# Optimization experiments

Hardware: AMD Instinct MI355X
Metric: run time of the kernel (lower is better)

## Reference

```python
import jax, jax.numpy as jnp
import numpy as np

# Model dims (Gemma-class)
B, T, HID = 1, 3072, 2048
H, KH, D = 16, 8, 128          # q heads, kv heads, head_dim
WIN = 1024                     # sliding window
EPS = 1e-6
SEQ = 1536                     # two packed sequences of length 1536


def _rms(x, w):
    # torch nn.RMSNorm: x * rsqrt(mean(x^2) + eps) [* weight]
    var = jnp.mean(x * x, axis=-1, keepdims=True)
    y = x * jax.lax.rsqrt(var + EPS)
    return y if w is None else y * w


def _rotate_half(x):
    x1, x2 = jnp.split(x, 2, axis=-1)
    return jnp.concatenate([-x2, x1], axis=-1)


def _rope(x, cos, sin):
    # x: [B,T,h,D]; cos/sin: [B,T,rd] -> unsqueeze head dim (matches cos.unsqueeze(2))
    c = cos[:, :, None, :]
    s = sin[:, :, None, :]
    rd = cos.shape[-1]
    xr, xp = x[..., :rd], x[..., rd:]
    xr = xr * c + _rotate_half(xr) * s
    return jnp.concatenate([xr, xp], axis=-1)


def _build_mask(cu_seqlens):
    # causal & within sliding window & same packed sequence (matches _sliding_mask)
    idx = jnp.arange(T)
    seg = jnp.searchsorted(cu_seqlens, idx, side='right') - 1
    i = idx[:, None]
    j = idx[None, :]
    return (i >= j) & ((i - j) < WIN) & (seg[:, None] == seg[None, :])


def _attn_layer(x, wq, qn, k, v, wo, cos, sin, mask):
    # x: [B,T,HID]; k,v: [T,KH,D] (possibly shared from an earlier layer)
    q = _rope(_rms((x @ wq).reshape(B, T, H, D), qn), cos, sin).reshape(T, H, D)
    rep = H // k.shape[1]
    kk = jnp.repeat(k, rep, axis=1)   # GQA: repeat_interleave over head dim
    vv = jnp.repeat(v, rep, axis=1)
    s = jnp.einsum('qhd,khd->hqk', q, kk)          # scale = 1.0 (as in source)
    s = jnp.where(mask, s, jnp.asarray(-1e30, s.dtype))
    p = jax.nn.softmax(s, axis=-1)
    o = jnp.einsum('hqk,khd->qhd', p, vv).reshape(B, T, H * D)
    return o @ wo


def setup_inputs() -> dict:
    key = jax.random.key(0)
    ks = jax.random.split(key, 10)
    hidden_states = jax.random.normal(ks[0], (B, T, HID), jnp.float32)
    # RoPE tables with per-packed-sequence position resets
    pos = jnp.concatenate([jnp.arange(SEQ), jnp.arange(SEQ)]).astype(jnp.float32)
    inv = 1.0 / (10000.0 ** (jnp.arange(0, D, 2, dtype=jnp.float32) / D))
    fr = pos[:, None] * inv[None, :]
    emb = jnp.concatenate([fr, fr], axis=-1)     # [T, D]
    cos = jnp.cos(emb)[None]                     # [1, T, D]
    sin = jnp.sin(emb)[None]
    w = lambda k, sh: 0.02 * jax.random.normal(k, sh, jnp.float32)
    return {
        'hidden_states': hidden_states,
        'cos': cos, 'sin': sin,
        'wq0': w(ks[1], (HID, H * D)), 'wk0': w(ks[2], (HID, KH * D)),
        'wv0': w(ks[3], (HID, KH * D)), 'wo0': w(ks[4], (H * D, HID)),
        'qn0': 1.0 + 0.01 * jax.random.normal(ks[5], (D,), jnp.float32),
        'kn0': 1.0 + 0.01 * jax.random.normal(ks[6], (D,), jnp.float32),
        'wq1': w(ks[7], (HID, H * D)), 'wo1': w(ks[8], (H * D, HID)),
        'qn1': 1.0 + 0.01 * jax.random.normal(ks[9], (D,), jnp.float32),
        'cu_seqlens': jnp.array([0, SEQ, T], dtype=jnp.int32),
    }


def reference(hidden_states, cos, sin, wq0, wk0, wv0, wo0, qn0, kn0, wq1, wo1, qn1, cu_seqlens):
    mask = _build_mask(cu_seqlens)
    # Layer 0: source layer -> computes and stores K/V
    k = _rope(_rms((hidden_states @ wk0).reshape(B, T, KH, D), kn0), cos, sin).reshape(T, KH, D)
    v = _rms((hidden_states @ wv0).reshape(B, T, KH, D), None).reshape(T, KH, D)
    out0 = _attn_layer(hidden_states, wq0, qn0, k, v, wo0, cos, sin, mask)
    # Layer 1: KV-shared layer -> reuses layer 0's K/V (skips k/v projections)
    out1 = _attn_layer(out0, wq1, qn1, k, v, wo1, cos, sin, mask)
    return out1
```

## Files before the change

kernel.cpp:

```cpp
#include <hip/hip_runtime.h>
#include <hip/hip_bf16.h>

#define T_TOK 3072
#define HIDDEN 2048
#define NHQ 16
#define NHKV 8
#define DH 128
#define WINDOW 1024
#define KVN 1024

typedef __attribute__((ext_vector_type(4))) float f32x4;
typedef __attribute__((ext_vector_type(8))) short bf16x8;
typedef __attribute__((ext_vector_type(8))) unsigned short ushort8;
typedef __attribute__((ext_vector_type(4))) unsigned short ushort4v;

__device__ __forceinline__ unsigned short f2bf(float f) {
  union { float fv; unsigned u; } v; v.fv = f;
  unsigned r = v.u + 0x7fffu + ((v.u >> 16) & 1u);
  return (unsigned short)(r >> 16);
}
__device__ __forceinline__ float bf2f(unsigned short h) {
  union { unsigned u; float f; } v; v.u = ((unsigned)h) << 16;
  return v.f;
}
__device__ __forceinline__ void split2(float f, unsigned short& hi, unsigned short& lo) {
  hi = f2bf(f);
  lo = f2bf(f - bf2f(hi));
}

__global__ __launch_bounds__(256) void prep(const float* __restrict__ hidden,
                                            const float* __restrict__ wq0,
                                            const float* __restrict__ wk0,
                                            const float* __restrict__ wv0,
                                            const float* __restrict__ wo0,
                                            const float* __restrict__ wq1,
                                            const float* __restrict__ wo1,
                                            unsigned short* __restrict__ xh,
                                            unsigned short* __restrict__ xl,
                                            unsigned short* __restrict__ wqkvh,
                                            unsigned short* __restrict__ wqkvl,
                                            unsigned short* __restrict__ wo0sh,
                                            unsigned short* __restrict__ wo0sl,
                                            unsigned short* __restrict__ wq1th,
                                            unsigned short* __restrict__ wq1tl,
                                            unsigned short* __restrict__ wo1th) {
  __shared__ float tile[32][33];
  const int K = HIDDEN;
  int id = blockIdx.x;
  if (id < 6144 || (id >= 14336 && id < 18432)) {
    const float* src; unsigned short *dh, *dl; int local;
    if (id < 6144) { src = hidden; dh = xh; dl = xl; local = id; }
    else           { src = wo0; dh = wo0sh; dl = wo0sl; local = id - 14336; }
    int i = (local * 256 + threadIdx.x) * 4;
    f32x4 v = *(const f32x4*)(src + i);
    ushort4v oh, ol;
#pragma unroll
    for (int j = 0; j < 4; ++j) {
      unsigned short h, l;
      split2(v[j], h, l);
      oh[j] = h; ol[j] = l;
    }
    *(ushort4v*)(dh + i) = oh;
    *(ushort4v*)(dl + i) = ol;
    return;
  }
  const float* W; int N, local; unsigned short *Dh, *Dl; size_t dstoff;
  if (id < 14336) {
    int lid = id - 6144;
    if (lid < 4096)      { W = wq0; N = 2048; local = lid;        dstoff = 0; }
    else if (lid < 6144) { W = wk0; N = 1024; local = lid - 4096; dstoff = (size_t)2048 * K; }
    else                 { W = wv0; N = 1024; local = lid - 6144; dstoff = (size_t)3072 * K; }
    Dh = wqkvh; Dl = wqkvl;
  } else if (id < 22528) {
    W = wq1; N = 2048; local = id - 18432; dstoff = 0;
    Dh = wq1th; Dl = wq1tl;
  } else {
    W = wo1; N = 2048; local = id - 22528; dstoff = 0;
    Dh = wo1th; Dl = nullptr;
  }
  int ntc = N / 32;
  int bn = (local % ntc) * 32, bk = (local / ntc) * 32;
  int tx = threadIdx.x & 31, ty = threadIdx.x >> 5;
#pragma unroll
  for (int i = 0; i < 4; ++i)
    tile[ty + i * 8][tx] = W[(size_t)(bk + ty + i * 8) * N + bn + tx];
  __syncthreads();
#pragma unroll
  for (int i = 0; i < 4; ++i) {
    unsigned short h, l;
    split2(tile[tx][ty + i * 8], h, l);
    Dh[dstoff + (size_t)(bn + ty + i * 8) * K + bk + tx] = h;
    if (Dl) Dl[dstoff + (size_t)(bn + ty + i * 8) * K + bk + tx] = l;
  }
}

__global__ __launch_bounds__(256) void transpose_u16(const unsigned short* __restrict__ src,
                                                     unsigned short* __restrict__ dst,
                                                     int R, int C) {
  __shared__ unsigned short tile[32][33];
  int bc = blockIdx.x * 32, br = blockIdx.y * 32;
  int tx = threadIdx.x & 31, ty = threadIdx.x >> 5;
#pragma unroll
  for (int i = 0; i < 4; ++i)
    tile[ty + i * 8][tx] = src[(size_t)(br + ty + i * 8) * C + bc + tx];
  __syncthreads();
#pragma unroll
  for (int i = 0; i < 4; ++i)
    dst[(size_t)(bc + ty + i * 8) * R + br + tx] = tile[tx][ty + i * 8];
}

#define GSLOT(lane) ((((lane) & 3) + 4 - (((lane) >> 3) & 3)) & 3)

__global__ __launch_bounds__(256) void gemm3_128(const unsigned short* __restrict__ Ah,
                                                 const unsigned short* __restrict__ Al,
                                                 const unsigned short* __restrict__ Bh,
                                                 const unsigned short* __restrict__ Bl,
                                                 float* __restrict__ Cq,
                                                 float* __restrict__ Ckv,
                                                 int strd, int M, int N, int K) {
  __shared__ unsigned short ah_lds[128 * 32];
  __shared__ unsigned short al_lds[128 * 32];
  __shared__ unsigned short bh_lds[128 * 32];
  __shared__ unsigned short bl_lds[128 * 32];
  const int tid = threadIdx.x, lane = tid & 63, wave = tid >> 6;
  const int wr = (wave >> 1) * 64, wc = (wave & 1) * 64;
  const int g = lane >> 4, r16 = lane & 15;
  int nwg = gridDim.x * gridDim.y;
  int id = blockIdx.y * gridDim.x + blockIdx.x;
  int nid = (id & 7) * (nwg >> 3) + (id >> 3);
  const int bm = nid % gridDim.x, bn = nid / gridDim.x;
  f32x4 acc[4][4];
#pragma unroll
  for (int i = 0; i < 4; ++i)
#pragma unroll
    for (int j = 0; j < 4; ++j) acc[i][j] = (f32x4){0.f, 0.f, 0.f, 0.f};

  const unsigned short* AhB = Ah + (size_t)bm * 128 * K;
  const unsigned short* AlB = Al + (size_t)bm * 128 * K;
  const unsigned short* BhB = Bh + (size_t)bn * 128 * K;
  const unsigned short* BlB = Bl + (size_t)bn * 128 * K;

  const int slg = GSLOT(lane) * 8;
  const int sr = ((r16 >> 1) & 3);

  for (int kt = 0; kt < K; kt += 32) {
    __syncthreads();
#pragma unroll
    for (int c = 0; c < 2; ++c) {
      size_t goff = (size_t)(wave * 32 + c * 16 + (lane >> 2)) * K + kt + slg;
      int loff = (wave * 2 + c) * 512;
      __builtin_amdgcn_global_load_lds(
          (const __attribute__((address_space(1))) unsigned int*)(AhB + goff),
          (__attribute__((address_space(3))) unsigned int*)(ah_lds + loff), 16, 0, 0);
      __builtin_amdgcn_global_load_lds(
          (const __attribute__((address_space(1))) unsigned int*)(AlB + goff),
          (__attribute__((address_space(3))) unsigned int*)(al_lds + loff), 16, 0, 0);
      __builtin_amdgcn_global_load_lds(
          (const __attribute__((address_space(1))) unsigned int*)(BhB + goff),
          (__attribute__((address_space(3))) unsigned int*)(bh_lds + loff), 16, 0, 0);
      __builtin_amdgcn_global_load_lds(
          (const __attribute__((address_space(1))) unsigned int*)(BlB + goff),
          (__attribute__((address_space(3))) unsigned int*)(bl_lds + loff), 16, 0, 0);
    }
    __syncthreads();
    bf16x8 ahf[4], alf[4], bhf[4], blf[4];
    int sa = ((g + sr) & 3) * 8;
#pragma unroll
    for (int i = 0; i < 4; ++i) {
      ahf[i] = *(const bf16x8*)&ah_lds[(wr + i * 16 + r16) * 32 + sa];
      alf[i] = *(const bf16x8*)&al_lds[(wr + i * 16 + r16) * 32 + sa];
      bhf[i] = *(const bf16x8*)&bh_lds[(wc + i * 16 + r16) * 32 + sa];
      blf[i] = *(const bf16x8*)&bl_lds[(wc + i * 16 + r16) * 32 + sa];
    }
#pragma unroll
    for (int i = 0; i < 4; ++i)
#pragma unroll
      for (int j = 0; j < 4; ++j) {
        acc[i][j] = __builtin_amdgcn_mfma_f32_16x16x32_bf16(ahf[i], bhf[j], acc[i][j], 0, 0, 0);
        acc[i][j] = __builtin_amdgcn_mfma_f32_16x16x32_bf16(ahf[i], blf[j], acc[i][j], 0, 0, 0);
        acc[i][j] = __builtin_amdgcn_mfma_f32_16x16x32_bf16(alf[i], bhf[j], acc[i][j], 0, 0, 0);
      }
  }

#pragma unroll
  for (int i = 0; i < 4; ++i) {
    int row = bm * 128 + wr + i * 16 + g * 4;
#pragma unroll
    for (int j = 0; j < 4; ++j) {
      int colg = bn * 128 + wc + j * 16 + r16;
      float* Cb; int cc;
      if (colg < 2048) { Cb = Cq; cc = colg; } else { Cb = Ckv; cc = colg - 2048; }
#pragma unroll
      for (int r = 0; r < 4; ++r)
        Cb[(size_t)(row + r) * strd + cc] = acc[i][j][r];
    }
  }
}

__global__ __launch_bounds__(256) void gemm3_64(const unsigned short* __restrict__ Ah,
                                                const unsigned short* __restrict__ Al,
                                                const unsigned short* __restrict__ Bh,
                                                const unsigned short* __restrict__ Bl,
                                                unsigned short* __restrict__ Ch,
                                                unsigned short* __restrict__ Cl,
                                                int M, int N, int K) {
  __shared__ unsigned short ah_lds[64 * 32];
  __shared__ unsigned short al_lds[64 * 32];
  __shared__ unsigned short bh_lds[128 * 32];
  __shared__ unsigned short bl_lds[128 * 32];
  const int tid = threadIdx.x, lane = tid & 63, wave = tid >> 6;
  const int wr = (wave >> 1) * 32, wc = (wave & 1) * 64;
  const int g = lane >> 4, r16 = lane & 15;
  int nwg = gridDim.x * gridDim.y;
  int id = blockIdx.y * gridDim.x + blockIdx.x;
  int nid = (id & 7) * (nwg >> 3) + (id >> 3);
  const int bm = nid % gridDim.x, bn = nid / gridDim.x;
  f32x4 acc[2][4];
#pragma unroll
  for (int i = 0; i < 2; ++i)
#pragma unroll
    for (int j = 0; j < 4; ++j) acc[i][j] = (f32x4){0.f, 0.f, 0.f, 0.f};

  const unsigned short* AhB = Ah + (size_t)bm * 64 * K;
  const unsigned short* AlB = Al + (size_t)bm * 64 * K;
  const unsigned short* BhB = Bh + (size_t)bn * 128 * K;
  const unsigned short* BlB = Bl + (size_t)bn * 128 * K;

  const int slg = GSLOT(lane) * 8;
  const int sr = ((r16 >> 1) & 3);

  for (int kt = 0; kt < K; kt += 32) {
    __syncthreads();
    {
      size_t goff = (size_t)(wave * 16 + (lane >> 2)) * K + kt + slg;
      __builtin_amdgcn_global_load_lds(
          (const __attribute__((address_space(1))) unsigned int*)(AhB + goff),
          (__attribute__((address_space(3))) unsigned int*)(ah_lds + wave * 512), 16, 0, 0);
      __builtin_amdgcn_global_load_lds(
          (const __attribute__((address_space(1))) unsigned int*)(AlB + goff),
          (__attribute__((address_space(3))) unsigned int*)(al_lds + wave * 512), 16, 0, 0);
    }
#pragma unroll
    for (int c = 0; c < 2; ++c) {
      size_t goff = (size_t)(wave * 32 + c * 16 + (lane >> 2)) * K + kt + slg;
      int loff = (wave * 2 + c) * 512;
      __builtin_amdgcn_global_load_lds(
          (const __attribute__((address_space(1))) unsigned int*)(BhB + goff),
          (__attribute__((address_space(3))) unsigned int*)(bh_lds + loff), 16, 0, 0);
      __builtin_amdgcn_global_load_lds(
          (const __attribute__((address_space(1))) unsigned int*)(BlB + goff),
          (__attribute__((address_space(3))) unsigned int*)(bl_lds + loff), 16, 0, 0);
    }
    __syncthreads();
    bf16x8 ahf[2], alf[2], bhf[4], blf[4];
    int sa = ((g + sr) & 3) * 8;
#pragma unroll
    for (int i = 0; i < 2; ++i) {
      ahf[i] = *(const bf16x8*)&ah_lds[(wr + i * 16 + r16) * 32 + sa];
      alf[i] = *(const bf16x8*)&al_lds[(wr + i * 16 + r16) * 32 + sa];
    }
#pragma unroll
    for (int j = 0; j < 4; ++j) {
      bhf[j] = *(const bf16x8*)&bh_lds[(wc + j * 16 + r16) * 32 + sa];
      blf[j] = *(const bf16x8*)&bl_lds[(wc + j * 16 + r16) * 32 + sa];
    }
#pragma unroll
    for (int i = 0; i < 2; ++i)
#pragma unroll
      for (int j = 0; j < 4; ++j) {
        acc[i][j] = __builtin_amdgcn_mfma_f32_16x16x32_bf16(ahf[i], bhf[j], acc[i][j], 0, 0, 0);
        acc[i][j] = __builtin_amdgcn_mfma_f32_16x16x32_bf16(ahf[i], blf[j], acc[i][j], 0, 0, 0);
        acc[i][j] = __builtin_amdgcn_mfma_f32_16x16x32_bf16(alf[i], bhf[j], acc[i][j], 0, 0, 0);
      }
  }

#pragma unroll
  for (int i = 0; i < 2; ++i) {
    int row = bm * 64 + wr + i * 16 + g * 4;
#pragma unroll
    for (int j = 0; j < 4; ++j) {
      int col = bn * 128 + wc + j * 16 + r16;
#pragma unroll
      for (int r = 0; r < 4; ++r) {
        unsigned short h, l;
        split2(acc[i][j][r], h, l);
        Ch[(size_t)(row + r) * N + col] = h;
        Cl[(size_t)(row + r) * N + col] = l;
      }
    }
  }
}

__global__ __launch_bounds__(256) void gemm3_96(const unsigned short* __restrict__ Ah,
                                                const unsigned short* __restrict__ Al,
                                                const unsigned short* __restrict__ Bh,
                                                const unsigned short* __restrict__ Bl,
                                                float* __restrict__ Cf,
                                                int M, int N, int K) {
  __shared__ unsigned short ah_lds[96 * 32];
  __shared__ unsigned short al_lds[96 * 32];
  __shared__ unsigned short bh_lds[128 * 32];
  __shared__ unsigned short bl_lds[128 * 32];
  const int tid = threadIdx.x, lane = tid & 63, wave = tid >> 6;
  const int wr = (wave >> 1) * 48, wc = (wave & 1) * 64;
  const int g = lane >> 4, r16 = lane & 15;
  int nwg = gridDim.x * gridDim.y;
  int id = blockIdx.y * gridDim.x + blockIdx.x;
  int nid = (id & 7) * (nwg >> 3) + (id >> 3);
  const int bm = nid % gridDim.x, bn = nid / gridDim.x;
  f32x4 acc[3][4];
#pragma unroll
  for (int i = 0; i < 3; ++i)
#pragma unroll
    for (int j = 0; j < 4; ++j) acc[i][j] = (f32x4){0.f, 0.f, 0.f, 0.f};

  const unsigned short* AhB = Ah + (size_t)bm * 96 * K;
  const unsigned short* AlB = Al + (size_t)bm * 96 * K;
  const unsigned short* BhB = Bh + (size_t)bn * 128 * K;
  const unsigned short* BlB = Bl + (size_t)bn * 128 * K;

  const int slg = GSLOT(lane) * 8;
  const int sr = ((r16 >> 1) & 3);

  for (int kt = 0; kt < K; kt += 32) {
    __syncthreads();
    {
      int c = wave;
      size_t goff = (size_t)(c * 16 + (lane >> 2)) * K + kt + slg;
      __builtin_amdgcn_global_load_lds(
          (const __attribute__((address_space(1))) unsigned int*)(AhB + goff),
          (__attribute__((address_space(3))) unsigned int*)(ah_lds + c * 512), 16, 0, 0);
      __builtin_amdgcn_global_load_lds(
          (const __attribute__((address_space(1))) unsigned int*)(AlB + goff),
          (__attribute__((address_space(3))) unsigned int*)(al_lds + c * 512), 16, 0, 0);
      if (wave < 2) {
        int c2 = 4 + wave;
        size_t goff2 = (size_t)(c2 * 16 + (lane >> 2)) * K + kt + slg;
        __builtin_amdgcn_global_load_lds(
            (const __attribute__((address_space(1))) unsigned int*)(AhB + goff2),
            (__attribute__((address_space(3))) unsigned int*)(ah_lds + c2 * 512), 16, 0, 0);
        __builtin_amdgcn_global_load_lds(
            (const __attribute__((address_space(1))) unsigned int*)(AlB + goff2),
            (__attribute__((address_space(3))) unsigned int*)(al_lds + c2 * 512), 16, 0, 0);
      }
    }
#pragma unroll
    for (int c = 0; c < 2; ++c) {
      size_t goff = (size_t)(wave * 32 + c * 16 + (lane >> 2)) * K + kt + slg;
      int loff = (wave * 2 + c) * 512;
      __builtin_amdgcn_global_load_lds(
          (const __attribute__((address_space(1))) unsigned int*)(BhB + goff),
          (__attribute__((address_space(3))) unsigned int*)(bh_lds + loff), 16, 0, 0);
      __builtin_amdgcn_global_load_lds(
          (const __attribute__((address_space(1))) unsigned int*)(BlB + goff),
          (__attribute__((address_space(3))) unsigned int*)(bl_lds + loff), 16, 0, 0);
    }
    __syncthreads();
    bf16x8 ahf[3], alf[3], bhf[4], blf[4];
    int sa = ((g + sr) & 3) * 8;
#pragma unroll
    for (int i = 0; i < 3; ++i) {
      ahf[i] = *(const bf16x8*)&ah_lds[(wr + i * 16 + r16) * 32 + sa];
      alf[i] = *(const bf16x8*)&al_lds[(wr + i * 16 + r16) * 32 + sa];
    }
#pragma unroll
    for (int j = 0; j < 4; ++j) {
      bhf[j] = *(const bf16x8*)&bh_lds[(wc + j * 16 + r16) * 32 + sa];
      blf[j] = *(const bf16x8*)&bl_lds[(wc + j * 16 + r16) * 32 + sa];
    }
#pragma unroll
    for (int i = 0; i < 3; ++i)
#pragma unroll
      for (int j = 0; j < 4; ++j) {
        acc[i][j] = __builtin_amdgcn_mfma_f32_16x16x32_bf16(ahf[i], bhf[j], acc[i][j], 0, 0, 0);
        acc[i][j] = __builtin_amdgcn_mfma_f32_16x16x32_bf16(ahf[i], blf[j], acc[i][j], 0, 0, 0);
        acc[i][j] = __builtin_amdgcn_mfma_f32_16x16x32_bf16(alf[i], bhf[j], acc[i][j], 0, 0, 0);
      }
  }

#pragma unroll
  for (int i = 0; i < 3; ++i) {
    int row = bm * 96 + wr + i * 16 + g * 4;
#pragma unroll
    for (int j = 0; j < 4; ++j) {
      int col = bn * 128 + wc + j * 16 + r16;
#pragma unroll
      for (int r = 0; r < 4; ++r)
        Cf[(size_t)(row + r) * N + col] = acc[i][j][r];
    }
  }
}

__global__ __launch_bounds__(256) void gemm1_96(const unsigned short* __restrict__ Ah,
                                                const unsigned short* __restrict__ Bh,
                                                float* __restrict__ Cf,
                                                int M, int N, int K) {
  __shared__ unsigned short ah_lds[96 * 32];
  __shared__ unsigned short bh_lds[128 * 32];
  const int tid = threadIdx.x, lane = tid & 63, wave = tid >> 6;
  const int wr = (wave >> 1) * 48, wc = (wave & 1) * 64;
  const int g = lane >> 4, r16 = lane & 15;
  int nwg = gridDim.x * gridDim.y;
  int id = blockIdx.y * gridDim.x + blockIdx.x;
  int nid = (id & 7) * (nwg >> 3) + (id >> 3);
  const int bm = nid % gridDim.x, bn = nid / gridDim.x;
  f32x4 acc[3][4];
#pragma unroll
  for (int i = 0; i < 3; ++i)
#pragma unroll
    for (int j = 0; j < 4; ++j) acc[i][j] = (f32x4){0.f, 0.f, 0.f, 0.f};

  const unsigned short* AhB = Ah + (size_t)bm * 96 * K;
  const unsigned short* BhB = Bh + (size_t)bn * 128 * K;

  const int slg = GSLOT(lane) * 8;
  const int sr = ((r16 >> 1) & 3);

  for (int kt = 0; kt < K; kt += 32) {
    __syncthreads();
    {
      int c = wave;
      size_t goff = (size_t)(c * 16 + (lane >> 2)) * K + kt + slg;
      __builtin_amdgcn_global_load_lds(
          (const __attribute__((address_space(1))) unsigned int*)(AhB + goff),
          (__attribute__((address_space(3))) unsigned int*)(ah_lds + c * 512), 16, 0, 0);
      if (wave < 2) {
        int c2 = 4 + wave;
        size_t goff2 = (size_t)(c2 * 16 + (lane >> 2)) * K + kt + slg;
        __builtin_amdgcn_global_load_lds(
            (const __attribute__((address_space(1))) unsigned int*)(AhB + goff2),
            (__attribute__((address_space(3))) unsigned int*)(ah_lds + c2 * 512), 16, 0, 0);
      }
    }
#pragma unroll
    for (int c = 0; c < 2; ++c) {
      size_t goff = (size_t)(wave * 32 + c * 16 + (lane >> 2)) * K + kt + slg;
      __builtin_amdgcn_global_load_lds(
          (const __attribute__((address_space(1))) unsigned int*)(BhB + goff),
          (__attribute__((address_space(3))) unsigned int*)(bh_lds + (wave * 2 + c) * 512), 16, 0, 0);
    }
    __syncthreads();
    bf16x8 ahf[3], bhf[4];
    int sa = ((g + sr) & 3) * 8;
#pragma unroll
    for (int i = 0; i < 3; ++i)
      ahf[i] = *(const bf16x8*)&ah_lds[(wr + i * 16 + r16) * 32 + sa];
#pragma unroll
    for (int j = 0; j < 4; ++j)
      bhf[j] = *(const bf16x8*)&bh_lds[(wc + j * 16 + r16) * 32 + sa];
#pragma unroll
    for (int i = 0; i < 3; ++i)
#pragma unroll
      for (int j = 0; j < 4; ++j)
        acc[i][j] = __builtin_amdgcn_mfma_f32_16x16x32_bf16(ahf[i], bhf[j], acc[i][j], 0, 0, 0);
  }

#pragma unroll
  for (int i = 0; i < 3; ++i) {
    int row = bm * 96 + wr + i * 16 + g * 4;
#pragma unroll
    for (int j = 0; j < 4; ++j) {
      int col = bn * 128 + wc + j * 16 + r16;
#pragma unroll
      for (int r = 0; r < 4; ++r)
        Cf[(size_t)(row + r) * N + col] = acc[i][j][r];
    }
  }
}

__global__ __launch_bounds__(256) void rms_kv(const float* __restrict__ X,
                                              const float* __restrict__ kn,
                                              const float* __restrict__ cosp,
                                              const float* __restrict__ sinp,
                                              unsigned short* __restrict__ kh,
                                              unsigned short* __restrict__ kl,
                                              unsigned short* __restrict__ vh) {
  const int half = T_TOK * NHKV / 4;
  bool isV = (int)blockIdx.x >= half;
  int bid = isV ? blockIdx.x - half : blockIdx.x;
  int row = bid * 4 + (threadIdx.x >> 6);
  int lane = threadIdx.x & 63;
  int t = row >> 3, hh_ = row & 7;
  const float* x = X + (size_t)t * HIDDEN + (isV ? KVN : 0) + (size_t)hh_ * DH;
  float x1 = x[lane], x2 = x[lane + 64];
  float ss = x1 * x1 + x2 * x2;
#pragma unroll
  for (int m = 1; m < 64; m <<= 1) ss += __shfl_xor(ss, m, 64);
  float inv = rsqrtf(ss * (1.0f / 128.0f) + 1e-6f);
  float y1 = x1 * inv, y2 = x2 * inv;
  if (!isV) {
    y1 *= kn[lane]; y2 *= kn[lane + 64];
    float c1 = cosp[t * DH + lane], s1 = sinp[t * DH + lane];
    float c2 = cosp[t * DH + lane + 64], s2 = sinp[t * DH + lane + 64];
    float o1 = y1 * c1 - y2 * s1;
    float o2 = y2 * c2 + y1 * s2;
    unsigned short h, l;
    split2(o1, h, l);
    kh[(size_t)row * DH + lane] = h;
    kl[(size_t)row * DH + lane] = l;
    split2(o2, h, l);
    kh[(size_t)row * DH + lane + 64] = h;
    kl[(size_t)row * DH + lane + 64] = l;
  } else {
    vh[(size_t)row * DH + lane] = f2bf(y1);
    vh[(size_t)row * DH + lane + 64] = f2bf(y2);
  }
}

template <int WRITE_LO>
__global__ __launch_bounds__(384) void attn3(const float* __restrict__ Qf,
                                             const float* __restrict__ qnw,
                                             const float* __restrict__ cosp,
                                             const float* __restrict__ sinp,
                                             const unsigned short* __restrict__ Kh,
                                             const unsigned short* __restrict__ Kl,
                                             const unsigned short* __restrict__ Vth,
                                             unsigned short* __restrict__ Oh,
                                             unsigned short* __restrict__ Ol,
                                             const int* __restrict__ cu, int ncu) {
  __shared__ unsigned short kh_lds[32][136];
  __shared__ unsigned short kl_lds[32][136];
  __shared__ unsigned short vh_lds[144][40];
  __shared__ unsigned short ph_lds[6][16][40];

  int id = blockIdx.y * gridDim.x + blockIdx.x;
  int xcd = id & 7;
  int j = id >> 3;
  int qt, h;
  if (j < 32) {
    qt = (j >> 1) + ((j & 1) << 4);
    h = 2 * xcd;
  } else {
    int k = 63 - j;
    qt = (k >> 1) + ((k & 1) << 4);
    h = 2 * xcd + 1;
  }
  const int qbase = qt * 96;
  const int kvh = h >> 1;
  const int tid = threadIdx.x, lane = tid & 63, wave = tid >> 6;
  const int g = lane >> 4, r16 = lane & 15;

  for (int i = tid; i < 16 * 40; i += 384) {
    int rr = i / 40, cc = i % 40;
    vh_lds[128 + rr][cc] = (rr == 0) ? (unsigned short)0x3F80 : (unsigned short)0;
  }

  bf16x8 aqh[4], aql[4];
  {
    int q_r = qbase + wave * 16 + r16;
    const float* xq = Qf + (size_t)q_r * HIDDEN + h * DH;
    float xv[4][8];
    float ss = 0.f;
#pragma unroll
    for (int ks = 0; ks < 4; ++ks) {
      f32x4 a = *(const f32x4*)(xq + ks * 32 + g * 8);
      f32x4 b = *(const f32x4*)(xq + ks * 32 + g * 8 + 4);
#pragma unroll
      for (int jj = 0; jj < 4; ++jj) { xv[ks][jj] = a[jj]; xv[ks][4 + jj] = b[jj]; }
#pragma unroll
      for (int jj = 0; jj < 8; ++jj) ss += xv[ks][jj] * xv[ks][jj];
    }
    ss += __shfl_xor(ss, 16, 64);
    ss += __shfl_xor(ss, 32, 64);
    float inv = rsqrtf(ss * (1.0f / 128.0f) + 1e-6f);
    float y[4][8];
#pragma unroll
    for (int ks = 0; ks < 4; ++ks) {
      f32x4 w0 = *(const f32x4*)(qnw + ks * 32 + g * 8);
      f32x4 w1 = *(const f32x4*)(qnw + ks * 32 + g * 8 + 4);
#pragma unroll
      for (int jj = 0; jj < 4; ++jj) {
        y[ks][jj] = xv[ks][jj] * inv * w0[jj];
        y[ks][4 + jj] = xv[ks][4 + jj] * inv * w1[jj];
      }
    }
    const float* cb = cosp + (size_t)q_r * DH;
    const float* sb = sinp + (size_t)q_r * DH;
#pragma unroll
    for (int ks = 0; ks < 4; ++ks) {
      bf16x8 th, tl;
#pragma unroll
      for (int j2 = 0; j2 < 2; ++j2) {
        int col = ks * 32 + g * 8 + j2 * 4;
        f32x4 cv = *(const f32x4*)(cb + col);
        f32x4 sv = *(const f32x4*)(sb + col);
#pragma unroll
        for (int jj = 0; jj < 4; ++jj) {
          float o;
          if (ks < 2) o = y[ks][j2 * 4 + jj] * cv[jj] - y[ks + 2][j2 * 4 + jj] * sv[jj];
          else        o = y[ks][j2 * 4 + jj] * cv[jj] + y[ks - 2][j2 * 4 + jj] * sv[jj];
          unsigned short hx, lx;
          split2(o, hx, lx);
          th[j2 * 4 + jj] = (short)hx;
          tl[j2 * 4 + jj] = (short)lx;
        }
      }
      aqh[ks] = th; aql[ks] = tl;
    }
  }

  int ssr[4];
#pragma unroll
  for (int r = 0; r < 4; ++r) {
    int q_r = qbase + wave * 16 + g * 4 + r;
    int s = 0;
    for (int i = 1; i < ncu; ++i) { int v = cu[i]; if (v <= q_r) s = v; }
    ssr[r] = s;
  }
  int ss_base = 0;
  for (int i = 1; i < ncu; ++i) { int v = cu[i]; if (v <= qbase) ss_base = v; }

  float m_r[4] = {-1e30f, -1e30f, -1e30f, -1e30f};
  f32x4 oacc[8];
#pragma unroll
  for (int db = 0; db < 8; ++db) oacc[db] = (f32x4){0.f, 0.f, 0.f, 0.f};
  f32x4 oaccL = (f32x4){0.f, 0.f, 0.f, 0.f};

  int lo = qbase - WINDOW + 1;
  if (lo < ss_base) lo = ss_base;
  if (lo < 0) lo = 0;
  int kt0 = lo & ~31;
  int ktend = qbase + 95;

  const bool stager = tid < 256;
  const int krow = (tid & 255) >> 3, kc = tid & 7;
  const int vd = (tid & 255) >> 1, vhalf = (tid & 1) * 16;
  const int qmin = qbase + wave * 16;
  const int sw0 = ((kc + 2 * (krow & 15)) & 15) * 16;
  const int sw1 = ((kc + 8 + 2 * (krow & 15)) & 15) * 16;

  ushort8 rkh0, rkh1, rkl0, rkl1, rvh0, rvh1;
  auto loadTile = [&](int kt) {
    if (!stager) return;
    size_t goff = ((size_t)(kt + krow) * NHKV + kvh) * DH + kc * 8;
    rkh0 = *(const ushort8*)(Kh + goff);
    rkh1 = *(const ushort8*)(Kh + goff + 64);
    rkl0 = *(const ushort8*)(Kl + goff);
    rkl1 = *(const ushort8*)(Kl + goff + 64);
    size_t voff = ((size_t)kvh * DH + vd) * T_TOK + kt + vhalf;
    rvh0 = *(const ushort8*)(Vth + voff);
    rvh1 = *(const ushort8*)(Vth + voff + 8);
  };
  auto writeTile = [&]() {
    if (!stager) return;
    char* kbh = (char*)&kh_lds[krow][0];
    char* kbl = (char*)&kl_lds[krow][0];
    *(ushort8*)(kbh + sw0) = rkh0;
    *(ushort8*)(kbh + sw1) = rkh1;
    *(ushort8*)(kbl + sw0) = rkl0;
    *(ushort8*)(kbl + sw1) = rkl1;
    *(ushort8*)&vh_lds[vd][vhalf] = rvh0;
    *(ushort8*)&vh_lds[vd][vhalf + 8] = rvh1;
  };

  loadTile(kt0);
  writeTile();
  __syncthreads();

  for (int kt = kt0; kt <= ktend; kt += 32) {
    const bool hasNext = (kt + 32 <= ktend);
    if (hasNext) loadTile(kt + 32);

    f32x4 s0 = (f32x4){0.f, 0.f, 0.f, 0.f}, s1 = (f32x4){0.f, 0.f, 0.f, 0.f};
    {
      const char* kb0h = (const char*)&kh_lds[r16][0];
      const char* kb1h = (const char*)&kh_lds[16 + r16][0];
      const char* kb0l = (const char*)&kl_lds[r16][0];
      const char* kb1l = (const char*)&kl_lds[16 + r16][0];
      __builtin_amdgcn_s_setprio(1);
#pragma unroll
      for (int ks = 0; ks < 4; ++ks) {
        int sl = ((ks * 4 + g + 2 * r16) & 15) * 16;
        bf16x8 bh0 = *(const bf16x8*)(kb0h + sl);
        bf16x8 bh1 = *(const bf16x8*)(kb1h + sl);
        bf16x8 bl0 = *(const bf16x8*)(kb0l + sl);
        bf16x8 bl1 = *(const bf16x8*)(kb1l + sl);
        s0 = __builtin_amdgcn_mfma_f32_16x16x32_bf16(aqh[ks], bh0, s0, 0, 0, 0);
        s0 = __builtin_amdgcn_mfma_f32_16x16x32_bf16(aqh[ks], bl0, s0, 0, 0, 0);
        s0 = __builtin_amdgcn_mfma_f32_16x16x32_bf16(aql[ks], bh0, s0, 0, 0, 0);
        s1 = __builtin_amdgcn_mfma_f32_16x16x32_bf16(aqh[ks], bh1, s1, 0, 0, 0);
        s1 = __builtin_amdgcn_mfma_f32_16x16x32_bf16(aqh[ks], bl1, s1, 0, 0, 0);
        s1 = __builtin_amdgcn_mfma_f32_16x16x32_bf16(aql[ks], bh1, s1, 0, 0, 0);
      }
      __builtin_amdgcn_s_setprio(0);
    }

    float sv0_[4], sv1_[4], mt_[4];
    bool ok0_[4], ok1_[4];
    bool interior = (kt + 31 <= qmin) && (kt >= qmin + 16 - WINDOW) &&
                    __all(kt >= ssr[3]);
    if (interior) {
#pragma unroll
      for (int r = 0; r < 4; ++r) {
        ok0_[r] = ok1_[r] = true;
        sv0_[r] = s0[r]; sv1_[r] = s1[r];
      }
    } else {
#pragma unroll
      for (int r = 0; r < 4; ++r) {
        int q_r = qmin + g * 4 + r;
        int k0 = kt + r16, k1 = k0 + 16;
        ok0_[r] = (k0 <= q_r) && (k0 > q_r - WINDOW) && (k0 >= ssr[r]);
        ok1_[r] = (k1 <= q_r) && (k1 > q_r - WINDOW) && (k1 >= ssr[r]);
        sv0_[r] = ok0_[r] ? s0[r] : -1e30f;
        sv1_[r] = ok1_[r] ? s1[r] : -1e30f;
      }
    }
#pragma unroll
    for (int r = 0; r < 4; ++r) {
      float mt = fmaxf(sv0_[r], sv1_[r]);
#pragma unroll
      for (int mm = 1; mm < 16; mm <<= 1) mt = fmaxf(mt, __shfl_xor(mt, mm, 64));
      mt_[r] = mt;
    }
    float grow = fmaxf(fmaxf(mt_[0] - m_r[0], mt_[1] - m_r[1]),
                       fmaxf(mt_[2] - m_r[2], mt_[3] - m_r[3]));
    if (!__all(grow <= 8.0f)) {
#pragma unroll
      for (int r = 0; r < 4; ++r) {
        float mnew = fmaxf(m_r[r], mt_[r]);
        float alpha = __expf(m_r[r] - mnew);
        m_r[r] = mnew;
#pragma unroll
        for (int db = 0; db < 8; ++db) oacc[db][r] *= alpha;
        oaccL[r] *= alpha;
      }
    }
#pragma unroll
    for (int r = 0; r < 4; ++r) {
      float p0v = ok0_[r] ? __expf(sv0_[r] - m_r[r]) : 0.f;
      float p1v = ok1_[r] ? __expf(sv1_[r] - m_r[r]) : 0.f;
      ph_lds[wave][g * 4 + r][r16] = f2bf(p0v);
      ph_lds[wave][g * 4 + r][16 + r16] = f2bf(p1v);
    }

    bf16x8 pah = *(const bf16x8*)&ph_lds[wave][r16][g * 8];
    __builtin_amdgcn_s_setprio(1);
#pragma unroll
    for (int db = 0; db < 8; ++db) {
      bf16x8 vfh = *(const bf16x8*)&vh_lds[db * 16 + r16][g * 8];
      oacc[db] = __builtin_amdgcn_mfma_f32_16x16x32_bf16(pah, vfh, oacc[db], 0, 0, 0);
    }
    {
      bf16x8 vfo = *(const bf16x8*)&vh_lds[128 + r16][g * 8];
      oaccL = __builtin_amdgcn_mfma_f32_16x16x32_bf16(pah, vfo, oaccL, 0, 0, 0);
    }
    __builtin_amdgcn_s_setprio(0);

    __syncthreads();
    if (hasNext) writeTile();
    __syncthreads();
  }

#pragma unroll
  for (int r = 0; r < 4; ++r) {
    int q_r = qbase + wave * 16 + g * 4 + r;
    float lsum = __shfl(oaccL[r], lane & 48, 64);
    float invl = 1.f / lsum;
#pragma unroll
    for (int db = 0; db < 8; ++db) {
      float ov = oacc[db][r] * invl;
      unsigned short hh, ll;
      split2(ov, hh, ll);
      Oh[(size_t)q_r * (NHQ * DH) + h * DH + db * 16 + r16] = hh;
      if (WRITE_LO) Ol[(size_t)q_r * (NHQ * DH) + h * DH + db * 16 + r16] = ll;
    }
  }
}

extern "C" void kernel_launch(void* const* d_in, const int* in_sizes, int n_in,
                              void* d_out, int out_size, void* d_ws, size_t ws_size,
                              hipStream_t stream) {
  const float* hidden = (const float*)d_in[0];
  const float* cosp   = (const float*)d_in[1];
  const float* sinp   = (const float*)d_in[2];
  const float* wq0    = (const float*)d_in[3];
  const float* wk0    = (const float*)d_in[4];
  const float* wv0    = (const float*)d_in[5];
  const float* wo0    = (const float*)d_in[6];
  const float* qn0    = (const float*)d_in[7];
  const float* kn0    = (const float*)d_in[8];
  const float* wq1    = (const float*)d_in[9];
  const float* wo1    = (const float*)d_in[10];
  const float* qn1    = (const float*)d_in[11];
  const int*   cu     = (const int*)d_in[12];
  int ncu = in_sizes[12];
  (void)n_in; (void)out_size; (void)ws_size;

  char* p = (char*)d_ws;
  auto alloc = [&](size_t bytes) { char* r = p; p += (bytes + 255) & ~255ull; return r; };

  unsigned short* wqkvh = (unsigned short*)alloc((size_t)2 * HIDDEN * HIDDEN * 2);
  unsigned short* wqkvl = (unsigned short*)alloc((size_t)2 * HIDDEN * HIDDEN * 2);
  unsigned short* wo0sh = (unsigned short*)alloc((size_t)HIDDEN * HIDDEN * 2);
  unsigned short* wo0sl = (unsigned short*)alloc((size_t)HIDDEN * HIDDEN * 2);
  unsigned short* wq1th = (unsigned short*)alloc((size_t)HIDDEN * HIDDEN * 2);
  unsigned short* wq1tl = (unsigned short*)alloc((size_t)HIDDEN * HIDDEN * 2);
  unsigned short* wo1t  = (unsigned short*)alloc((size_t)HIDDEN * HIDDEN * 2);
  float*          c32q  = (float*)alloc((size_t)T_TOK * HIDDEN * 4);
  float*          c32kv = (float*)alloc((size_t)T_TOK * HIDDEN * 4);
  unsigned short* xh    = (unsigned short*)alloc((size_t)T_TOK * HIDDEN * 2);
  unsigned short* xl    = (unsigned short*)alloc((size_t)T_TOK * HIDDEN * 2);
  unsigned short* kh    = (unsigned short*)alloc((size_t)T_TOK * KVN * 2);
  unsigned short* kl    = (unsigned short*)alloc((size_t)T_TOK * KVN * 2);
  unsigned short* vh    = (unsigned short*)alloc((size_t)T_TOK * KVN * 2);
  unsigned short* vth   = (unsigned short*)alloc((size_t)T_TOK * KVN * 2);

  unsigned short* W01th = (unsigned short*)c32q;
  unsigned short* W01tl = W01th + (size_t)HIDDEN * HIDDEN;

  prep<<<26624, 256, 0, stream>>>(hidden, wq0, wk0, wv0, wo0, wq1, wo1,
                                  xh, xl, wqkvh, wqkvl, wo0sh, wo0sl, wq1th, wq1tl, wo1t);

  gemm3_128<<<dim3(T_TOK / 128, 4096 / 128), 256, 0, stream>>>(
      xh, xl, wqkvh, wqkvl, c32q, c32kv, HIDDEN, T_TOK, 4096, HIDDEN);

  rms_kv<<<2 * T_TOK * NHKV / 4, 256, 0, stream>>>(c32kv, kn0, cosp, sinp, kh, kl, vh);
  transpose_u16<<<dim3(KVN / 32, T_TOK / 32), 256, 0, stream>>>(vh, vth, T_TOK, KVN);

  attn3<1><<<dim3(32, 16), 384, 0, stream>>>(c32q, qn0, cosp, sinp, kh, kl, vth, xh, xl, cu, ncu);

  gemm3_64<<<dim3(HIDDEN / 64, HIDDEN / 128), 256, 0, stream>>>(
      wq1th, wq1tl, wo0sh, wo0sl, W01th, W01tl, HIDDEN, HIDDEN, HIDDEN);

  gemm3_96<<<dim3(T_TOK / 96, HIDDEN / 128), 256, 0, stream>>>(
      xh, xl, W01th, W01tl, c32kv, T_TOK, HIDDEN, HIDDEN);

  attn3<0><<<dim3(32, 16), 384, 0, stream>>>(c32kv, qn1, cosp, sinp, kh, kl, vth, xh, nullptr, cu, ncu);

  gemm1_96<<<dim3(T_TOK / 96, HIDDEN / 128), 256, 0, stream>>>(xh, wo1t, (float*)d_out, T_TOK, HIDDEN, HIDDEN);
}
```

Measured before the change: 603.1 us.

## Merge QKV projection GEMM and W01 weight-product GEMM into one launch

Fuses the QKV projection GEMM (768 tiles) and the weight-only Wq1·Wo0 product GEMM (512 tiles) into a single kernel that picks its branch from the block index. This fills the tail of the QKV grid with independent work and removes one launch. W01 now gets its own workspace buffer instead of aliasing c32q, because both run at the same time. Shared LDS is sized for the larger branch, which may lower occupancy for the smaller one.

```diff
diff --git a/kernel.cpp b/kernel.cpp
--- a/kernel.cpp
+++ b/kernel.cpp
@@ -111,181 +111,178 @@
 
 #define GSLOT(lane) ((((lane) & 3) + 4 - (((lane) >> 3) & 3)) & 3)
 
-__global__ __launch_bounds__(256) void gemm3_128(const unsigned short* __restrict__ Ah,
-                                                 const unsigned short* __restrict__ Al,
-                                                 const unsigned short* __restrict__ Bh,
-                                                 const unsigned short* __restrict__ Bl,
-                                                 float* __restrict__ Cq,
-                                                 float* __restrict__ Ckv,
-                                                 int strd, int M, int N, int K) {
-  __shared__ unsigned short ah_lds[128 * 32];
-  __shared__ unsigned short al_lds[128 * 32];
-  __shared__ unsigned short bh_lds[128 * 32];
-  __shared__ unsigned short bl_lds[128 * 32];
+__global__ __launch_bounds__(256) void gemm_qkv_w01(
+    const unsigned short* __restrict__ Ah,
+    const unsigned short* __restrict__ Al,
+    const unsigned short* __restrict__ Bh,
+    const unsigned short* __restrict__ Bl,
+    float* __restrict__ Cq, float* __restrict__ Ckv,
+    const unsigned short* __restrict__ Wah,
+    const unsigned short* __restrict__ Wal,
+    const unsigned short* __restrict__ Wbh,
+    const unsigned short* __restrict__ Wbl,
+    unsigned short* __restrict__ Ch, unsigned short* __restrict__ Cl) {
+  __shared__ unsigned short lds[16384];
   const int tid = threadIdx.x, lane = tid & 63, wave = tid >> 6;
-  const int wr = (wave >> 1) * 64, wc = (wave & 1) * 64;
   const int g = lane >> 4, r16 = lane & 15;
-  int nwg = gridDim.x * gridDim.y;
-  int id = blockIdx.y * gridDim.x + blockIdx.x;
-  int nid = (id & 7) * (nwg >> 3) + (id >> 3);
-  const int bm = nid % gridDim.x, bn = nid / gridDim.x;
-  f32x4 acc[4][4];
-#pragma unroll
-  for (int i = 0; i < 4; ++i)
-#pragma unroll
-    for (int j = 0; j < 4; ++j) acc[i][j] = (f32x4){0.f, 0.f, 0.f, 0.f};
-
-  const unsigned short* AhB = Ah + (size_t)bm * 128 * K;
-  const unsigned short* AlB = Al + (size_t)bm * 128 * K;
-  const unsigned short* BhB = Bh + (size_t)bn * 128 * K;
-  const unsigned short* BlB = Bl + (size_t)bn * 128 * K;
-
   const int slg = GSLOT(lane) * 8;
   const int sr = ((r16 >> 1) & 3);
-
-  for (int kt = 0; kt < K; kt += 32) {
-    __syncthreads();
-#pragma unroll
-    for (int c = 0; c < 2; ++c) {
-      size_t goff = (size_t)(wave * 32 + c * 16 + (lane >> 2)) * K + kt + slg;
-      int loff = (wave * 2 + c) * 512;
-      __builtin_amdgcn_global_load_lds(
-          (const __attribute__((address_space(1))) unsigned int*)(AhB + goff),
-          (__attribute__((address_space(3))) unsigned int*)(ah_lds + loff), 16, 0, 0);
-      __builtin_amdgcn_global_load_lds(
-          (const __attribute__((address_space(1))) unsigned int*)(AlB + goff),
-          (__attribute__((address_space(3))) unsigned int*)(al_lds + loff), 16, 0, 0);
-      __builtin_amdgcn_global_load_lds(
-          (const __attribute__((address_space(1))) unsigned int*)(BhB + goff),
-          (__attribute__((address_space(3))) unsigned int*)(bh_lds + loff), 16, 0, 0);
-      __builtin_amdgcn_global_load_lds(
-          (const __attribute__((address_space(1))) unsigned int*)(BlB + goff),
-          (__attribute__((address_space(3))) unsigned int*)(bl_lds + loff), 16, 0, 0);
-    }
-    __syncthreads();
-    bf16x8 ahf[4], alf[4], bhf[4], blf[4];
-    int sa = ((g + sr) & 3) * 8;
+  int id = blockIdx.x;
+
+  if (id < 768) {
+    const int K = HIDDEN;
+    unsigned short* ah_lds = lds;
+    unsigned short* al_lds = lds + 4096;
+    unsigned short* bh_lds = lds + 8192;
+    unsigned short* bl_lds = lds + 12288;
+    const int wr = (wave >> 1) * 64, wc = (wave & 1) * 64;
+    int nid = (id & 7) * 96 + (id >> 3);
+    const int bm = nid % 24, bn = nid / 24;
+    f32x4 acc[4][4];
+#pragma unroll
+    for (int i = 0; i < 4; ++i)
+#pragma unroll
+      for (int j = 0; j < 4; ++j) acc[i][j] = (f32x4){0.f, 0.f, 0.f, 0.f};
+
+    const unsigned short* AhB = Ah + (size_t)bm * 128 * K;
+    const unsigned short* AlB = Al + (size_t)bm * 128 * K;
+    const unsigned short* BhB = Bh + (size_t)bn * 128 * K;
+    const unsigned short* BlB = Bl + (size_t)bn * 128 * K;
+
+    for (int kt = 0; kt < K; kt += 32) {
+      __syncthreads();
+#pragma unroll
+      for (int c = 0; c < 2; ++c) {
+        size_t goff = (size_t)(wave * 32 + c * 16 + (lane >> 2)) * K + kt + slg;
+        int loff = (wave * 2 + c) * 512;
+        __builtin_amdgcn_global_load_lds(
+            (const __attribute__((address_space(1))) unsigned int*)(AhB + goff),
+            (__attribute__((address_space(3))) unsigned int*)(ah_lds + loff), 16, 0, 0);
+        __builtin_amdgcn_global_load_lds(
+            (const __attribute__((address_space(1))) unsigned int*)(AlB + goff),
+            (__attribute__((address_space(3))) unsigned int*)(al_lds + loff), 16, 0, 0);
+        __builtin_amdgcn_global_load_lds(
+            (const __attribute__((address_space(1))) unsigned int*)(BhB + goff),
+            (__attribute__((address_space(3))) unsigned int*)(bh_lds + loff), 16, 0, 0);
+        __builtin_amdgcn_global_load_lds(
+            (const __attribute__((address_space(1))) unsigned int*)(BlB + goff),
+            (__attribute__((address_space(3))) unsigned int*)(bl_lds + loff), 16, 0, 0);
+      }
+      __syncthreads();
+      bf16x8 ahf[4], alf[4], bhf[4], blf[4];
+      int sa = ((g + sr) & 3) * 8;
+#pragma unroll
+      for (int i = 0; i < 4; ++i) {
+        ahf[i] = *(const bf16x8*)&ah_lds[(wr + i * 16 + r16) * 32 + sa];
+        alf[i] = *(const bf16x8*)&al_lds[(wr + i * 16 + r16) * 32 + sa];
+        bhf[i] = *(const bf16x8*)&bh_lds[(wc + i * 16 + r16) * 32 + sa];
+        blf[i] = *(const bf16x8*)&bl_lds[(wc + i * 16 + r16) * 32 + sa];
+      }
+#pragma unroll
+      for (int i = 0; i < 4; ++i)
+#pragma unroll
+        for (int j = 0; j < 4; ++j) {
+          acc[i][j] = __builtin_amdgcn_mfma_f32_16x16x32_bf16(ahf[i], bhf[j], acc[i][j], 0, 0, 0);
+          acc[i][j] = __builtin_amdgcn_mfma_f32_16x16x32_bf16(ahf[i], blf[j], acc[i][j], 0, 0, 0);
+          acc[i][j] = __builtin_amdgcn_mfma_f32_16x16x32_bf16(alf[i], bhf[j], acc[i][j], 0, 0, 0);
+        }
+    }
+
 #pragma unroll
     for (int i = 0; i < 4; ++i) {
-      ahf[i] = *(const bf16x8*)&ah_lds[(wr + i * 16 + r16) * 32 + sa];
-      alf[i] = *(const bf16x8*)&al_lds[(wr + i * 16 + r16) * 32 + sa];
-      bhf[i] = *(const bf16x8*)&bh_lds[(wc + i * 16 + r16) * 32 + sa];
-      blf[i] = *(const bf16x8*)&bl_lds[(wc + i * 16 + r16) * 32 + sa];
-    }
-#pragma unroll
-    for (int i = 0; i < 4; ++i)
+      int row = bm * 128 + wr + i * 16 + g * 4;
 #pragma unroll
       for (int j = 0; j < 4; ++j) {
-        acc[i][j] = __builtin_amdgcn_mfma_f32_16x16x32_bf16(ahf[i], bhf[j], acc[i][j], 0, 0, 0);
-        acc[i][j] = __builtin_amdgcn_mfma_f32_16x16x32_bf16(ahf[i], blf[j], acc[i][j], 0, 0, 0);
-        acc[i][j] = __builtin_amdgcn_mfma_f32_16x16x32_bf16(alf[i], bhf[j], acc[i][j], 0, 0, 0);
-      }
-  }
-
-#pragma unroll
-  for (int i = 0; i < 4; ++i) {
-    int row = bm * 128 + wr + i * 16 + g * 4;
-#pragma unroll
-    for (int j = 0; j < 4; ++j) {
-      int colg = bn * 128 + wc + j * 16 + r16;
-      float* Cb; int cc;
-      if (colg < 2048) { Cb = Cq; cc = colg; } else { Cb = Ckv; cc = colg - 2048; }
-#pragma unroll
-      for (int r = 0; r < 4; ++r)
-        Cb[(size_t)(row + r) * strd + cc] = acc[i][j][r];
-    }
-  }
-}
-
-__global__ __launch_bounds__(256) void gemm3_64(const unsigned short* __restrict__ Ah,
-                                                const unsigned short* __restrict__ Al,
-                                                const unsigned short* __restrict__ Bh,
-                                                const unsigned short* __restrict__ Bl,
-                                                unsigned short* __restrict__ Ch,
-                                                unsigned short* __restrict__ Cl,
-                                                int M, int N, int K) {
-  __shared__ unsigned short ah_lds[64 * 32];
-  __shared__ unsigned short al_lds[64 * 32];
-  __shared__ unsigned short bh_lds[128 * 32];
-  __shared__ unsigned short bl_lds[128 * 32];
-  const int tid = threadIdx.x, lane = tid & 63, wave = tid >> 6;
-  const int wr = (wave >> 1) * 32, wc = (wave & 1) * 64;
-  const int g = lane >> 4, r16 = lane & 15;
-  int nwg = gridDim.x * gridDim.y;
-  int id = blockIdx.y * gridDim.x + blockIdx.x;
-  int nid = (id & 7) * (nwg >> 3) + (id >> 3);
-  const int bm = nid % gridDim.x, bn = nid / gridDim.x;
-  f32x4 acc[2][4];
-#pragma unroll
-  for (int i = 0; i < 2; ++i)
-#pragma unroll
-    for (int j = 0; j < 4; ++j) acc[i][j] = (f32x4){0.f, 0.f, 0.f, 0.f};
-
-  const unsigned short* AhB = Ah + (size_t)bm * 64 * K;
-  const unsigned short* AlB = Al + (size_t)bm * 64 * K;
-  const unsigned short* BhB = Bh + (size_t)bn * 128 * K;
-  const unsigned short* BlB = Bl + (size_t)bn * 128 * K;
-
-  const int slg = GSLOT(lane) * 8;
-  const int sr = ((r16 >> 1) & 3);
-
-  for (int kt = 0; kt < K; kt += 32) {
-    __syncthreads();
-    {
-      size_t goff = (size_t)(wave * 16 + (lane >> 2)) * K + kt + slg;
-      __builtin_amdgcn_global_load_lds(
-          (const __attribute__((address_space(1))) unsigned int*)(AhB + goff),
-          (__attribute__((address_space(3))) unsigned int*)(ah_lds + wave * 512), 16, 0, 0);
-      __builtin_amdgcn_global_load_lds(
-          (const __attribute__((address_space(1))) unsigned int*)(AlB + goff),
-          (__attribute__((address_space(3))) unsigned int*)(al_lds + wave * 512), 16, 0, 0);
-    }
-#pragma unroll
-    for (int c = 0; c < 2; ++c) {
-      size_t goff = (size_t)(wave * 32 + c * 16 + (lane >> 2)) * K + kt + slg;
-      int loff = (wave * 2 + c) * 512;
-      __builtin_amdgcn_global_load_lds(
-          (const __attribute__((address_space(1))) unsigned int*)(BhB + goff),
-          (__attribute__((address_space(3))) unsigned int*)(bh_lds + loff), 16, 0, 0);
-      __builtin_amdgcn_global_load_lds(
-          (const __attribute__((address_space(1))) unsigned int*)(BlB + goff),
-          (__attribute__((address_space(3))) unsigned int*)(bl_lds + loff), 16, 0, 0);
-    }
-    __syncthreads();
-    bf16x8 ahf[2], alf[2], bhf[4], blf[4];
-    int sa = ((g + sr) & 3) * 8;
+        int colg = bn * 128 + wc + j * 16 + r16;
+        float* Cb; int cc;
+        if (colg < 2048) { Cb = Cq; cc = colg; } else { Cb = Ckv; cc = colg - 2048; }
+#pragma unroll
+        for (int r = 0; r < 4; ++r)
+          Cb[(size_t)(row + r) * HIDDEN + cc] = acc[i][j][r];
+      }
+    }
+    return;
+  }
+
+  {
+    const int K = HIDDEN;
+    unsigned short* ah_lds = lds;
+    unsigned short* al_lds = lds + 2048;
+    unsigned short* bh_lds = lds + 4096;
+    unsigned short* bl_lds = lds + 8192;
+    const int wr = (wave >> 1) * 32, wc = (wave & 1) * 64;
+    int lid = id - 768;
+    int nid = (lid & 7) * 64 + (lid >> 3);
+    const int bm = nid % 32, bn = nid / 32;
+    f32x4 acc[2][4];
+#pragma unroll
+    for (int i = 0; i < 2; ++i)
+#pragma unroll
+      for (int j = 0; j < 4; ++j) acc[i][j] = (f32x4){0.f, 0.f, 0.f, 0.f};
+
+    const unsigned short* AhB = Wah + (size_t)bm * 64 * K;
+    const unsigned short* AlB = Wal + (size_t)bm * 64 * K;
+    const unsigned short* BhB = Wbh + (size_t)bn * 128 * K;
+    const unsigned short* BlB = Wbl + (size_t)bn * 128 * K;
+
+    for (int kt = 0; kt < K; kt += 32) {
+      __syncthreads();
+      {
+        size_t goff = (size_t)(wave * 16 + (lane >> 2)) * K + kt + slg;
+        __builtin_amdgcn_global_load_lds(
+            (const __attribute__((address_space(1))) unsigned int*)(AhB + goff),
+            (__attribute__((address_space(3))) unsigned int*)(ah_lds + wave * 512), 16, 0, 0);
+        __builtin_amdgcn_global_load_lds(
+            (const __attribute__((address_space(1))) unsigned int*)(AlB + goff),
+            (__attribute__((address_space(3))) unsigned int*)(al_lds + wave * 512), 16, 0, 0);
+      }
+#pragma unroll
+      for (int c = 0; c < 2; ++c) {
+        size_t goff = (size_t)(wave * 32 + c * 16 + (lane >> 2)) * K + kt + slg;
+        int loff = (wave * 2 + c) * 512;
+        __builtin_amdgcn_global_load_lds(
+            (const __attribute__((address_space(1))) unsigned int*)(BhB + goff),
+            (__attribute__((address_space(3))) unsigned int*)(bh_lds + loff), 16, 0, 0);
+        __builtin_amdgcn_global_load_lds(
+            (const __attribute__((address_space(1))) unsigned int*)(BlB + goff),
+            (__attribute__((address_space(3))) unsigned int*)(bl_lds + loff), 16, 0, 0);
+      }
+      __syncthreads();
+      bf16x8 ahf[2], alf[2], bhf[4], blf[4];
+      int sa = ((g + sr) & 3) * 8;
+#pragma unroll
+      for (int i = 0; i < 2; ++i) {
+        ahf[i] = *(const bf16x8*)&ah_lds[(wr + i * 16 + r16) * 32 + sa];
+        alf[i] = *(const bf16x8*)&al_lds[(wr + i * 16 + r16) * 32 + sa];
+      }
+#pragma unroll
+      for (int j = 0; j < 4; ++j) {
+        bhf[j] = *(const bf16x8*)&bh_lds[(wc + j * 16 + r16) * 32 + sa];
+        blf[j] = *(const bf16x8*)&bl_lds[(wc + j * 16 + r16) * 32 + sa];
+      }
+#pragma unroll
+      for (int i = 0; i < 2; ++i)
+#pragma unroll
+        for (int j = 0; j < 4; ++j) {
+          acc[i][j] = __builtin_amdgcn_mfma_f32_16x16x32_bf16(ahf[i], bhf[j], acc[i][j], 0, 0, 0);
+          acc[i][j] = __builtin_amdgcn_mfma_f32_16x16x32_bf16(ahf[i], blf[j], acc[i][j], 0, 0, 0);
+          acc[i][j] = __builtin_amdgcn_mfma_f32_16x16x32_bf16(alf[i], bhf[j], acc[i][j], 0, 0, 0);
+        }
+    }
+
 #pragma unroll
     for (int i = 0; i < 2; ++i) {
-      ahf[i] = *(const bf16x8*)&ah_lds[(wr + i * 16 + r16) * 32 + sa];
-      alf[i] = *(const bf16x8*)&al_lds[(wr + i * 16 + r16) * 32 + sa];
-    }
-#pragma unroll
-    for (int j = 0; j < 4; ++j) {
-      bhf[j] = *(const bf16x8*)&bh_lds[(wc + j * 16 + r16) * 32 + sa];
-      blf[j] = *(const bf16x8*)&bl_lds[(wc + j * 16 + r16) * 32 + sa];
-    }
-#pragma unroll
-    for (int i = 0; i < 2; ++i)
+      int row = bm * 64 + wr + i * 16 + g * 4;
 #pragma unroll
       for (int j = 0; j < 4; ++j) {
-        acc[i][j] = __builtin_amdgcn_mfma_f32_16x16x32_bf16(ahf[i], bhf[j], acc[i][j], 0, 0, 0);
-        acc[i][j] = __builtin_amdgcn_mfma_f32_16x16x32_bf16(ahf[i], blf[j], acc[i][j], 0, 0, 0);
-        acc[i][j] = __builtin_amdgcn_mfma_f32_16x16x32_bf16(alf[i], bhf[j], acc[i][j], 0, 0, 0);
-      }
-  }
-
-#pragma unroll
-  for (int i = 0; i < 2; ++i) {
-    int row = bm * 64 + wr + i * 16 + g * 4;
-#pragma unroll
-    for (int j = 0; j < 4; ++j) {
-      int col = bn * 128 + wc + j * 16 + r16;
-#pragma unroll
-      for (int r = 0; r < 4; ++r) {
-        unsigned short h, l;
-        split2(acc[i][j][r], h, l);
-        Ch[(size_t)(row + r) * N + col] = h;
-        Cl[(size_t)(row + r) * N + col] = l;
+        int col = bn * 128 + wc + j * 16 + r16;
+#pragma unroll
+        for (int r = 0; r < 4; ++r) {
+          unsigned short h, l;
+          split2(acc[i][j][r], h, l);
+          Ch[(size_t)(row + r) * HIDDEN + col] = h;
+          Cl[(size_t)(row + r) * HIDDEN + col] = l;
+        }
       }
     }
   }
@@ -797,6 +794,8 @@
   unsigned short* wq1th = (unsigned short*)alloc((size_t)HIDDEN * HIDDEN * 2);
   unsigned short* wq1tl = (unsigned short*)alloc((size_t)HIDDEN * HIDDEN * 2);
   unsigned short* wo1t  = (unsigned short*)alloc((size_t)HIDDEN * HIDDEN * 2);
+  unsigned short* W01th = (unsigned short*)alloc((size_t)HIDDEN * HIDDEN * 2);
+  unsigned short* W01tl = (unsigned short*)alloc((size_t)HIDDEN * HIDDEN * 2);
   float*          c32q  = (float*)alloc((size_t)T_TOK * HIDDEN * 4);
   float*          c32kv = (float*)alloc((size_t)T_TOK * HIDDEN * 4);
   unsigned short* xh    = (unsigned short*)alloc((size_t)T_TOK * HIDDEN * 2);
@@ -806,23 +805,18 @@
   unsigned short* vh    = (unsigned short*)alloc((size_t)T_TOK * KVN * 2);
   unsigned short* vth   = (unsigned short*)alloc((size_t)T_TOK * KVN * 2);
 
-  unsigned short* W01th = (unsigned short*)c32q;
-  unsigned short* W01tl = W01th + (size_t)HIDDEN * HIDDEN;
-
   prep<<<26624, 256, 0, stream>>>(hidden, wq0, wk0, wv0, wo0, wq1, wo1,
                                   xh, xl, wqkvh, wqkvl, wo0sh, wo0sl, wq1th, wq1tl, wo1t);
 
-  gemm3_128<<<dim3(T_TOK / 128, 4096 / 128), 256, 0, stream>>>(
-      xh, xl, wqkvh, wqkvl, c32q, c32kv, HIDDEN, T_TOK, 4096, HIDDEN);
+  gemm_qkv_w01<<<1280, 256, 0, stream>>>(
+      xh, xl, wqkvh, wqkvl, c32q, c32kv,
+      wq1th, wq1tl, wo0sh, wo0sl, W01th, W01tl);
 
   rms_kv<<<2 * T_TOK * NHKV / 4, 256, 0, stream>>>(c32kv, kn0, cosp, sinp, kh, kl, vh);
   transpose_u16<<<dim3(KVN / 32, T_TOK / 32), 256, 0, stream>>>(vh, vth, T_TOK, KVN);
 
   attn3<1><<<dim3(32, 16), 384, 0, stream>>>(c32q, qn0, cosp, sinp, kh, kl, vth, xh, xl, cu, ncu);
 
-  gemm3_64<<<dim3(HIDDEN / 64, HIDDEN / 128), 256, 0, stream>>>(
-      wq1th, wq1tl, wo0sh, wo0sl, W01th, W01tl, HIDDEN, HIDDEN, HIDDEN);
-
   gemm3_96<<<dim3(T_TOK / 96, HIDDEN / 128), 256, 0, stream>>>(
       xh, xl, W01th, W01tl, c32kv, T_TOK, HIDDEN, HIDDEN);
 
```

After: 606.9 us. About the same (+0.6%).
